# Performance work log

Measured on AMD Instinct MI355X. Metric: run time of the kernel, lower is better.

Reference implementation:

```python
import jax, jax.numpy as jnp
import numpy as np

T, N, C, D, S = 512, 32, 1296, 512, 30
NORM_SCALE = 32.0
NEGINF = -1e9


def setup_inputs() -> dict:
    key = jax.random.key(0)
    k1, k2, k3, k4, k5 = jax.random.split(key, 5)
    feats = jax.random.normal(k1, (T * N, D), dtype=jnp.float32)
    classifier_weight = jax.random.normal(k2, (D, C), dtype=jnp.float32)
    labeling = jax.random.randint(k3, (N, S), 1, C)  # targets cannot be blank(0)
    logit_lgts = (T - jax.random.randint(k4, (N,), 0, 32)).astype(jnp.int32)
    labeling_lgts = (S - jax.random.randint(k5, (N,), 0, 5)).astype(jnp.int32)
    return dict(feats=feats, classifier_weight=classifier_weight,
                labeling=labeling, logit_lgts=logit_lgts, labeling_lgts=labeling_lgts)


def _ctc_loss(log_probs, labels, in_lens, lab_lens):
    # log_probs: (T, N, C); labels: (N, S); blank = 0; reduction = 'sum'
    Tt, Nn, Cc = log_probs.shape
    Ss = labels.shape[1]
    L = 2 * Ss + 1
    # extended labeling: blank, l1, blank, l2, ..., blank  -> (N, L)
    ext = jnp.zeros((Nn, L), dtype=labels.dtype).at[:, 1::2].set(labels)
    # gather per-state log-probs: (T, N, L)
    lp_ext = jnp.take_along_axis(log_probs, jnp.broadcast_to(ext[None], (Tt, Nn, L)), axis=2)
    # skip transition s-2 -> s allowed iff s > 1 and ext[s] != ext[s-2]
    skip_ok = jnp.concatenate(
        [jnp.zeros((Nn, 2), dtype=bool), ext[:, 2:] != ext[:, :-2]], axis=1)
    alpha0 = (jnp.full((Nn, L), NEGINF, dtype=log_probs.dtype)
              .at[:, 0].set(lp_ext[0, :, 0])
              .at[:, 1].set(lp_ext[0, :, 1]))

    def step(alpha, inp):
        lp_t, t = inp  # lp_t: (N, L)
        a1 = alpha
        a2 = jnp.pad(alpha[:, :-1], ((0, 0), (1, 0)), constant_values=NEGINF)
        a3 = jnp.where(skip_ok,
                       jnp.pad(alpha[:, :-2], ((0, 0), (2, 0)), constant_values=NEGINF),
                       NEGINF)
        new = jax.nn.logsumexp(jnp.stack([a1, a2, a3], axis=0), axis=0) + lp_t
        # freeze alpha once t reaches a sample's input length
        alpha = jnp.where((t < in_lens)[:, None], new, alpha)
        return alpha, None

    alpha, _ = jax.lax.scan(step, alpha0, (lp_ext[1:], jnp.arange(1, Tt)))
    Ln = 2 * lab_lens + 1  # (N,)
    last = jnp.take_along_axis(alpha, (Ln - 1)[:, None], axis=1)[:, 0]
    last2 = jnp.take_along_axis(alpha, (Ln - 2)[:, None], axis=1)[:, 0]
    nll = -jnp.logaddexp(last, last2)
    return jnp.sum(nll)


def reference(feats, classifier_weight, labeling, logit_lgts, labeling_lgts):
    # RadialCTC: cosine logits with norm_scale, then CTC on log-softmax.
    w_n = classifier_weight / jnp.linalg.norm(classifier_weight, axis=0, keepdims=True)  # (D, C)
    f_n = feats / jnp.linalg.norm(feats, axis=1, keepdims=True)  # (T*N, D)
    logits = NORM_SCALE * (f_n @ w_n)  # (T*N, C)
    log_probs = jax.nn.log_softmax(logits.reshape(T, N, C), axis=-1)
    return _ctc_loss(log_probs, labeling, logit_lgts, labeling_lgts)
```

## Files before the change

### kernel.cpp

```cpp
#include <hip/hip_runtime.h>
#include <stdint.h>
#include <stddef.h>


typedef _Float16 f16;
typedef _Float16 f16x8 __attribute__((ext_vector_type(8)));
typedef float f32x4 __attribute__((ext_vector_type(4)));
typedef __attribute__((address_space(1))) void* as1_void_ptr;
typedef __attribute__((address_space(3))) void* as3_void_ptr;

#define TT 512
#define NN 32
#define CC 1296
#define DD 512
#define SS 30
#define CP 1408
#define LL 61
#define NEGINF (-1e9f)
#define NORM_SCALE 32.0f
#define LOG2E 1.4426950408889634f
#define LN2   0.6931471805599453f

__device__ __forceinline__ float fexp2(float x) { return __builtin_amdgcn_exp2f(x); }
__device__ __forceinline__ float flog2(float x) { return __builtin_amdgcn_logf(x); }

__device__ __forceinline__ float dpp_sr1_neginf(float x) {
    return __int_as_float(__builtin_amdgcn_update_dpp(
        __float_as_int(NEGINF), __float_as_int(x), 0x138, 0xF, 0xF, false));
}

__global__ void colnorm_kernel(const float* __restrict__ W, float* __restrict__ ssq) {
    int c = blockIdx.x * 64 + threadIdx.x;
    if (c >= CC) return;
    int d0 = blockIdx.y * 64;
    float ss = 0.f;
    #pragma unroll 8
    for (int d = d0; d < d0 + 64; ++d) {
        float v = W[(size_t)d * CC + c];
        ss += v * v;
    }
    atomicAdd(&ssq[c], ss);
}

__global__ void wt_kernel(const float* __restrict__ W, const float* __restrict__ ssq,
                          f16* __restrict__ wt) {
    int idx = blockIdx.x * 256 + threadIdx.x;
    int c = idx >> 9, d = idx & 511;
    float v = 0.f;
    if (c < CC) v = W[(size_t)d * CC + c] * rsqrtf(ssq[c]);
    wt[idx] = (f16)v;
}

__global__ __launch_bounds__(256) void fnorm_kernel(const float* __restrict__ feats,
                                                    f16* __restrict__ fn) {
    int wv = (blockIdx.x * 256 + threadIdx.x) >> 6;
    int lane = threadIdx.x & 63;
    const float4* src = (const float4*)(feats + (size_t)wv * DD) + lane * 2;
    float4 a = src[0], b = src[1];
    float ss = a.x*a.x + a.y*a.y + a.z*a.z + a.w*a.w
             + b.x*b.x + b.y*b.y + b.z*b.z + b.w*b.w;
    #pragma unroll
    for (int off = 32; off; off >>= 1) ss += __shfl_xor(ss, off);
    float r = rsqrtf(ss);
    f16x8 o;
    o[0]=(f16)(a.x*r); o[1]=(f16)(a.y*r); o[2]=(f16)(a.z*r); o[3]=(f16)(a.w*r);
    o[4]=(f16)(b.x*r); o[5]=(f16)(b.y*r); o[6]=(f16)(b.z*r); o[7]=(f16)(b.w*r);
    *(f16x8*)(fn + (size_t)wv * DD + lane * 8) = o;
}

__global__ __launch_bounds__(256) void gemm_sumexp_kernel(const f16* __restrict__ A,
                                                          const f16* __restrict__ B,
                                                          float* __restrict__ sumexp) {
    __shared__ __align__(16) f16 As[128 * 32];
    __shared__ __align__(16) f16 Bs[128 * 32];
    int bm = blockIdx.x, bn = blockIdx.y;
    int tid = threadIdx.x;
    int w = tid >> 6, lane = tid & 63;
    int wm = w >> 1, wn = w & 1;
    int lm = lane & 15, hi = lane >> 4;
    f32x4 acc[4][4];
    f32x4 zero = {0.f, 0.f, 0.f, 0.f};
    #pragma unroll
    for (int i = 0; i < 4; ++i)
        #pragma unroll
        for (int j = 0; j < 4; ++j) acc[i][j] = zero;

    for (int kb = 0; kb < 16; ++kb) {
        #pragma unroll
        for (int p = 0; p < 2; ++p) {
            int s = p * 256 + tid;
            int row = s >> 2, ch = s & 3;
            const f16* ga = A + (size_t)(bm * 128 + row) * DD + kb * 32 + ch * 8;
            const f16* gb = B + (size_t)(bn * 128 + row) * DD + kb * 32 + ch * 8;
            __builtin_amdgcn_global_load_lds((as1_void_ptr)ga,
                (as3_void_ptr)&As[(p * 256 + w * 64) * 8], 16, 0, 0);
            __builtin_amdgcn_global_load_lds((as1_void_ptr)gb,
                (as3_void_ptr)&Bs[(p * 256 + w * 64) * 8], 16, 0, 0);
        }
        __syncthreads();
        f16x8 af[4], bf[4];
        #pragma unroll
        for (int i = 0; i < 4; ++i)
            af[i] = *(const f16x8*)&As[(wm * 64 + i * 16 + lm) * 32 + hi * 8];
        #pragma unroll
        for (int j = 0; j < 4; ++j)
            bf[j] = *(const f16x8*)&Bs[(wn * 64 + j * 16 + lm) * 32 + hi * 8];
        #pragma unroll
        for (int i = 0; i < 4; ++i)
            #pragma unroll
            for (int j = 0; j < 4; ++j)
                acc[i][j] = __builtin_amdgcn_mfma_f32_16x16x32_f16(af[i], bf[j], acc[i][j], 0, 0, 0);
        __syncthreads();
    }
    #pragma unroll
    for (int i = 0; i < 4; ++i) {
        float rs[4] = {0.f, 0.f, 0.f, 0.f};
        #pragma unroll
        for (int j = 0; j < 4; ++j) {
            int c = bn * 128 + wn * 64 + j * 16 + lm;
            bool ok = (c < CC);
            #pragma unroll
            for (int r = 0; r < 4; ++r)
                rs[r] += ok ? fexp2(acc[i][j][r] * (NORM_SCALE * LOG2E)) : 0.f;
        }
        #pragma unroll
        for (int off = 1; off < 16; off <<= 1) {
            #pragma unroll
            for (int r = 0; r < 4; ++r) rs[r] += __shfl_xor(rs[r], off);
        }
        if (lm == 0) {
            int rowb = bm * 128 + wm * 64 + i * 16 + hi * 4;
            #pragma unroll
            for (int r = 0; r < 4; ++r) atomicAdd(&sumexp[rowb + r], rs[r]);
        }
    }
}

__global__ __launch_bounds__(256) void gather_kernel(const f16* __restrict__ fn,
                                                     const f16* __restrict__ wt,
                                                     const float* __restrict__ sumexp,
                                                     const int* __restrict__ labels,
                                                     float* __restrict__ lp_lab) {
    __shared__ __align__(16) f16 Bs[16 * 32 * 32];
    __shared__ __align__(16) f16 As[64 * 32];
    __shared__ float ls2[64];
    int n = blockIdx.x, t0 = blockIdx.y * 64;
    int tid = threadIdx.x;
    int w = tid >> 6, lane = tid & 63;
    int lm = lane & 15, hi = lane >> 4;

    #pragma unroll
    for (int it = 0; it < 8; ++it) {
        int s = it * 256 + tid;
        int row = (s >> 2) & 31;
        int cls = (row == 0 || row > SS) ? 0 : labels[n * SS + row - 1];
        const f16* gb = wt + (size_t)cls * DD + (s >> 7) * 32 + (s & 3) * 8;
        __builtin_amdgcn_global_load_lds((as1_void_ptr)gb,
            (as3_void_ptr)&Bs[(it * 256 + w * 64) * 8], 16, 0, 0);
    }
    if (tid < 64) ls2[tid] = flog2(sumexp[(size_t)(t0 + tid) * NN + n]);

    f32x4 acc[2];
    acc[0] = (f32x4){0.f, 0.f, 0.f, 0.f};
    acc[1] = (f32x4){0.f, 0.f, 0.f, 0.f};
    for (int kb = 0; kb < 16; ++kb) {
        int row = tid >> 2, ch = tid & 3;
        const f16* ga = fn + (size_t)((t0 + row) * NN + n) * DD + kb * 32 + ch * 8;
        __builtin_amdgcn_global_load_lds((as1_void_ptr)ga,
            (as3_void_ptr)&As[(w * 64) * 8], 16, 0, 0);
        __syncthreads();
        f16x8 af = *(const f16x8*)&As[(w * 16 + lm) * 32 + hi * 8];
        f16x8 bf0 = *(const f16x8*)&Bs[kb * 1024 + lm * 32 + hi * 8];
        f16x8 bf1 = *(const f16x8*)&Bs[kb * 1024 + (16 + lm) * 32 + hi * 8];
        acc[0] = __builtin_amdgcn_mfma_f32_16x16x32_f16(af, bf0, acc[0], 0, 0, 0);
        acc[1] = __builtin_amdgcn_mfma_f32_16x16x32_f16(af, bf1, acc[1], 0, 0, 0);
        __syncthreads();
    }
    #pragma unroll
    for (int jn = 0; jn < 2; ++jn) {
        int j = jn * 16 + lm;
        if (j >= 31) continue;
        float* dst = lp_lab + ((size_t)n * 31 + j) * TT + t0;
        #pragma unroll
        for (int r = 0; r < 4; ++r) {
            int tl = w * 16 + hi * 4 + r;
            dst[tl] = acc[jn][r] * (NORM_SCALE * LOG2E) - ls2[tl];
        }
    }
}

__global__ void ctc_kernel(const float* __restrict__ lp_lab, const int* __restrict__ labels,
                           const int* __restrict__ in_lens, const int* __restrict__ lab_lens,
                           float* __restrict__ nll) {
    int n = blockIdx.x;
    int s = threadIdx.x;
    bool valid = s < LL;
    int ext = (valid && (s & 1)) ? labels[n * SS + (s >> 1)] : 0;
    int jmap = (valid && (s & 1)) ? ((s >> 1) + 1) : 0;
    int ext2 = __shfl_up(ext, 2);
    bool skip = (s >= 2) && valid && (ext != ext2);
    int Tin = in_lens[n];
    const float4* lp4 = (const float4*)(lp_lab + ((size_t)n * 31 + jmap) * TT);

    float4 cur = lp4[0];
    float4 nxt = lp4[1];
    float4 nx2 = lp4[2];
    float alpha = (s <= 1) ? cur.x : NEGINF;

    auto step = [&](int t, float lp) {
        float a2 = dpp_sr1_neginf(alpha);
        float a3 = dpp_sr1_neginf(a2);
        a3 = skip ? a3 : NEGINF;
        float m = fmaxf(alpha, fmaxf(a2, a3));
        float sum = fexp2(alpha - m) + fexp2(a2 - m) + fexp2(a3 - m);
        float nv = m + flog2(sum) + lp;
        if (t < Tin) alpha = nv;
    };

    step(1, cur.y); step(2, cur.z); step(3, cur.w);
    for (int g = 1; g < 128; ++g) {
        cur = nxt; nxt = nx2;
        if (g + 2 < 128) nx2 = lp4[g + 2];
        step(4 * g + 0, cur.x);
        step(4 * g + 1, cur.y);
        step(4 * g + 2, cur.z);
        step(4 * g + 3, cur.w);
    }

    int Ln = 2 * lab_lens[n] + 1;
    float last  = __shfl(alpha, Ln - 1);
    float last2 = __shfl(alpha, Ln - 2);
    float m2 = fmaxf(last, last2);
    float v = -(m2 + flog2(fexp2(last - m2) + fexp2(last2 - m2))) * LN2;
    if (s == 0) nll[n] = v;
}

__global__ void reduce_kernel(const float* __restrict__ nll, float* __restrict__ out) {
    int s = threadIdx.x;
    float v = (s < NN) ? nll[s] : 0.f;
    #pragma unroll
    for (int off = 32; off; off >>= 1) v += __shfl_xor(v, off);
    if (s == 0) out[0] = v;
}

extern "C" void kernel_launch(void* const* d_in, const int* in_sizes, int n_in,
                              void* d_out, int out_size, void* d_ws, size_t ws_size,
                              hipStream_t stream) {
    const float* feats        = (const float*)d_in[0];
    const float* W            = (const float*)d_in[1];
    const int*   labeling     = (const int*)d_in[2];
    const int*   logit_lgts   = (const int*)d_in[3];
    const int*   labeling_lgts= (const int*)d_in[4];
    float* out = (float*)d_out;
    char* ws = (char*)d_ws;

    size_t off = 0;
    f16*   wt     = (f16*)(ws + off);   off += (size_t)CP * DD * 2;
    f16*   fn     = (f16*)(ws + off);   off += (size_t)TT * NN * DD * 2;
    float* ssq    = (float*)(ws + off); off += 1312 * 4;
    float* sumexp = (float*)(ws + off); off += (size_t)TT * NN * 4;
    float* lp_lab = (float*)(ws + off); off += (size_t)NN * 31 * TT * 4;
    float* nllb   = (float*)(ws + off); off += 64 * 4;

    hipMemsetAsync(ssq, 0, 1312 * 4, stream);
    hipMemsetAsync(sumexp, 0, (size_t)TT * NN * 4, stream);

    colnorm_kernel<<<dim3((CC + 63) / 64, 8), 64, 0, stream>>>(W, ssq);
    wt_kernel<<<(CP * DD) / 256, 256, 0, stream>>>(W, ssq, wt);
    fnorm_kernel<<<(TT * NN) / 4, 256, 0, stream>>>(feats, fn);
    gemm_sumexp_kernel<<<dim3(TT * NN / 128, CP / 128), 256, 0, stream>>>(fn, wt, sumexp);
    gather_kernel<<<dim3(NN, TT / 64), 256, 0, stream>>>(fn, wt, sumexp, labeling, lp_lab);
    ctc_kernel<<<NN, 64, 0, stream>>>(lp_lab, labeling, logit_lgts, labeling_lgts, nllb);
    reduce_kernel<<<1, 64, 0, stream>>>(nllb, out);

    (void)in_sizes; (void)n_in; (void)out_size; (void)ws_size;
}
```

Baseline: 169.6 us.

## Prefetch full A tile in gather kernel and two-step the CTC recurrence per exchange

The gather kernel now loads the whole 64x512 feature tile into LDS up front with one barrier, instead of a load/sync/compute/sync loop over 16 k-blocks. The CTC kernel advances two time steps per cross-lane exchange: each lane computes the intermediate alphas for itself and its two left neighbours redundantly, then does four DPP shifts per pair of steps, halving the serial dependency chain of shuffles. This adds redundant exp/log work, extra global loads of neighbouring label rows, and more LDS usage in the gather kernel, which may lower occupancy.

```diff
diff --git a/kernel.cpp b/kernel.cpp
--- a/kernel.cpp
+++ b/kernel.cpp
@@ -142,7 +142,7 @@
                                                      const int* __restrict__ labels,
                                                      float* __restrict__ lp_lab) {
     __shared__ __align__(16) f16 Bs[16 * 32 * 32];
-    __shared__ __align__(16) f16 As[64 * 32];
+    __shared__ __align__(16) f16 As[16 * 64 * 32];
     __shared__ float ls2[64];
     int n = blockIdx.x, t0 = blockIdx.y * 64;
     int tid = threadIdx.x;
@@ -158,23 +158,27 @@
         __builtin_amdgcn_global_load_lds((as1_void_ptr)gb,
             (as3_void_ptr)&Bs[(it * 256 + w * 64) * 8], 16, 0, 0);
     }
+    #pragma unroll
+    for (int it = 0; it < 16; ++it) {
+        int s = it * 256 + tid;
+        int kb = s >> 8, row = (s >> 2) & 63, ch = s & 3;
+        const f16* ga = fn + (size_t)((t0 + row) * NN + n) * DD + kb * 32 + ch * 8;
+        __builtin_amdgcn_global_load_lds((as1_void_ptr)ga,
+            (as3_void_ptr)&As[(it * 256 + w * 64) * 8], 16, 0, 0);
+    }
     if (tid < 64) ls2[tid] = flog2(sumexp[(size_t)(t0 + tid) * NN + n]);
+    __syncthreads();
 
     f32x4 acc[2];
     acc[0] = (f32x4){0.f, 0.f, 0.f, 0.f};
     acc[1] = (f32x4){0.f, 0.f, 0.f, 0.f};
+    #pragma unroll
     for (int kb = 0; kb < 16; ++kb) {
-        int row = tid >> 2, ch = tid & 3;
-        const f16* ga = fn + (size_t)((t0 + row) * NN + n) * DD + kb * 32 + ch * 8;
-        __builtin_amdgcn_global_load_lds((as1_void_ptr)ga,
-            (as3_void_ptr)&As[(w * 64) * 8], 16, 0, 0);
-        __syncthreads();
-        f16x8 af = *(const f16x8*)&As[(w * 16 + lm) * 32 + hi * 8];
+        f16x8 af  = *(const f16x8*)&As[kb * 2048 + (w * 16 + lm) * 32 + hi * 8];
         f16x8 bf0 = *(const f16x8*)&Bs[kb * 1024 + lm * 32 + hi * 8];
         f16x8 bf1 = *(const f16x8*)&Bs[kb * 1024 + (16 + lm) * 32 + hi * 8];
         acc[0] = __builtin_amdgcn_mfma_f32_16x16x32_f16(af, bf0, acc[0], 0, 0, 0);
         acc[1] = __builtin_amdgcn_mfma_f32_16x16x32_f16(af, bf1, acc[1], 0, 0, 0);
-        __syncthreads();
     }
     #pragma unroll
     for (int jn = 0; jn < 2; ++jn) {
@@ -198,38 +202,66 @@
     int ext = (valid && (s & 1)) ? labels[n * SS + (s >> 1)] : 0;
     int jmap = (valid && (s & 1)) ? ((s >> 1) + 1) : 0;
     int ext2 = __shfl_up(ext, 2);
-    bool skip = (s >= 2) && valid && (ext != ext2);
+    bool skip0 = (s >= 2) && valid && (ext != ext2);
+    int sk = skip0 ? 1 : 0;
+    bool skip1 = (s >= 1) && __shfl_up(sk, 1);
+    bool skip2 = (s >= 2) && __shfl_up(sk, 2);
+    int jm1 = (s >= 1) ? __shfl_up(jmap, 1) : 0;
+    int jm2 = (s >= 2) ? __shfl_up(jmap, 2) : 0;
     int Tin = in_lens[n];
-    const float4* lp4 = (const float4*)(lp_lab + ((size_t)n * 31 + jmap) * TT);
-
-    float4 cur = lp4[0];
-    float4 nxt = lp4[1];
-    float4 nx2 = lp4[2];
-    float alpha = (s <= 1) ? cur.x : NEGINF;
-
-    auto step = [&](int t, float lp) {
-        float a2 = dpp_sr1_neginf(alpha);
-        float a3 = dpp_sr1_neginf(a2);
-        a3 = skip ? a3 : NEGINF;
-        float m = fmaxf(alpha, fmaxf(a2, a3));
-        float sum = fexp2(alpha - m) + fexp2(a2 - m) + fexp2(a3 - m);
-        float nv = m + flog2(sum) + lp;
-        if (t < Tin) alpha = nv;
+    const float4* g0 = (const float4*)(lp_lab + ((size_t)n * 31 + jmap) * TT);
+    const float4* g1 = (const float4*)(lp_lab + ((size_t)n * 31 + jm1) * TT);
+    const float4* g2 = (const float4*)(lp_lab + ((size_t)n * 31 + jm2) * TT);
+
+    auto lse3 = [](float x, float y, float z) {
+        float m = fmaxf(x, fmaxf(y, z));
+        return m + flog2(fexp2(x - m) + fexp2(y - m) + fexp2(z - m)); };
+
+    float4 c0 = g0[0], c1 = g1[0], c2 = g2[0];
+    float4 n0 = g0[1], n1 = g1[1], n2 = g2[1];
+    float4 x0 = g0[2], x1 = g1[2], x2 = g2[2];
+
+    float a0 = (s <= 1)           ? c0.x : NEGINF;
+    float a1 = (s == 1 || s == 2) ? c1.x : NEGINF;
+    float a2 = (s == 2 || s == 3) ? c2.x : NEGINF;
+    float l3 = __shfl_up(c0.x, 3), l4 = __shfl_up(c0.x, 4);
+    float a3 = (s == 3 || s == 4) ? l3 : NEGINF;
+    float a4 = (s == 4 || s == 5) ? l4 : NEGINF;
+
+    auto pair2 = [&](int t, float lA0, float lA1, float lA2, float lB0) {
+        float p0 = lse3(a0, a1, skip0 ? a2 : NEGINF) + lA0;
+        float p1 = lse3(a1, a2, skip1 ? a3 : NEGINF) + lA1;
+        float p2 = lse3(a2, a3, skip2 ? a4 : NEGINF) + lA2;
+        if (t >= Tin) { p0 = a0; p1 = a1; p2 = a2; }
+        float m0 = lse3(p0, p1, skip0 ? p2 : NEGINF) + lB0;
+        if (t + 1 >= Tin) m0 = p0;
+        a0 = m0;
+        a1 = dpp_sr1_neginf(a0);
+        a2 = dpp_sr1_neginf(a1);
+        a3 = dpp_sr1_neginf(a2);
+        a4 = dpp_sr1_neginf(a3);
     };
 
-    step(1, cur.y); step(2, cur.z); step(3, cur.w);
+    {
+        float p0 = lse3(a0, a1, skip0 ? a2 : NEGINF) + c0.y;
+        a0 = p0;
+        a1 = dpp_sr1_neginf(a0);
+        a2 = dpp_sr1_neginf(a1);
+        a3 = dpp_sr1_neginf(a2);
+        a4 = dpp_sr1_neginf(a3);
+    }
+    pair2(2, c0.z, c1.z, c2.z, c0.w);
     for (int g = 1; g < 128; ++g) {
-        cur = nxt; nxt = nx2;
-        if (g + 2 < 128) nx2 = lp4[g + 2];
-        step(4 * g + 0, cur.x);
-        step(4 * g + 1, cur.y);
-        step(4 * g + 2, cur.z);
-        step(4 * g + 3, cur.w);
+        c0 = n0; c1 = n1; c2 = n2;
+        n0 = x0; n1 = x1; n2 = x2;
+        if (g + 2 < 128) { x0 = g0[g + 2]; x1 = g1[g + 2]; x2 = g2[g + 2]; }
+        pair2(4 * g,     c0.x, c1.x, c2.x, c0.y);
+        pair2(4 * g + 2, c0.z, c1.z, c2.z, c0.w);
     }
 
     int Ln = 2 * lab_lens[n] + 1;
-    float last  = __shfl(alpha, Ln - 1);
-    float last2 = __shfl(alpha, Ln - 2);
+    float last  = __shfl(a0, Ln - 1);
+    float last2 = __shfl(a0, Ln - 2);
     float m2 = fmaxf(last, last2);
     float v = -(m2 + flog2(fexp2(last - m2) + fexp2(last2 - m2))) * LN2;
     if (s == 0) nll[n] = v;
```

New measurement: 183.1 us. 1.08x slower.
